# Kernel tuning notes

Measured on AMD Instinct MI355X. Metric: run time of the kernel, lower is better.

Reference implementation:

```python
import jax, jax.numpy as jnp
import numpy as np

B, S, H, DH, W, G, M = 2, 4096, 12, 64, 256, 64, 256
D = H * DH  # 768
VOCAB = 50282
NEG = -1e9


def setup_inputs() -> dict:
    key = jax.random.key(0)
    ks = jax.random.split(key, 16)
    f = lambda k, shp, s=0.02: jax.random.normal(k, shp, jnp.float32) * s
    return {
        'input_ids': jax.random.randint(ks[0], (B, S), 0, VOCAB, jnp.int32),
        'attn_mask': jnp.ones((B, S), jnp.float32),
        'html_idx': jnp.sort(jax.random.randint(ks[1], (B, M), 0, S, jnp.int32), axis=-1),
        'embed': f(ks[2], (VOCAB, D), 1.0),
        'Wq': f(ks[3], (D, D)), 'bq': jnp.zeros((D,), jnp.float32),
        'Wk': f(ks[4], (D, D)), 'bk': jnp.zeros((D,), jnp.float32),
        'Wv': f(ks[5], (D, D)), 'bv': jnp.zeros((D,), jnp.float32),
        'Wo': f(ks[6], (D, D)), 'bo': jnp.zeros((D,), jnp.float32),
        'gamma': jnp.ones((D,), jnp.float32), 'beta': jnp.zeros((D,), jnp.float32),
        'Wp': f(ks[7], (D, D)), 'bp': jnp.zeros((D,), jnp.float32),
        'Wa': f(ks[8], (D, 3)), 'ba': jnp.zeros((3,), jnp.float32),
        'Ws': f(ks[9], (D, 2)), 'bs': jnp.zeros((2,), jnp.float32),
    }


def _band_shift(t, n_chunks):
    # t: [..., n_chunks+2, W, ...chunked along axis -3/-2]; gather 3 neighbor chunks
    return jnp.concatenate([t[..., i:i + n_chunks, :, :] for i in range(3)], axis=-2)


def longformer_hpt(input_ids, attn_mask, html_idx, embed, Wq, bq, Wk, bk, Wv, bv,
                   Wo, bo, gamma, beta, Wp, bp, Wa, ba, Ws, bs):
    x = embed[input_ids]  # [B,S,D]
    heads = lambda t: t.reshape(B, S, H, DH).transpose(0, 2, 1, 3)  # [B,H,S,DH]
    q, k, v = heads(x @ Wq + bq), heads(x @ Wk + bk), heads(x @ Wv + bv)
    scale = 1.0 / np.sqrt(DH).astype(np.float32)
    C = S // W  # chunks

    # --- sliding-window (banded) attention, one-sided window W ---
    kp = jnp.pad(k, ((0, 0), (0, 0), (W, W), (0, 0))).reshape(B, H, C + 2, W, DH)
    vp = jnp.pad(v, ((0, 0), (0, 0), (W, W), (0, 0))).reshape(B, H, C + 2, W, DH)
    k3 = _band_shift(kp, C)  # [B,H,C,3W,DH]
    v3 = _band_shift(vp, C)
    qc = q.reshape(B, H, C, W, DH)
    sb = jnp.einsum('bhcqd,bhckd->bhcqk', qc, k3) * scale  # [B,H,C,W,3W]

    ii = jnp.arange(W)[:, None]
    jj = jnp.arange(3 * W)[None, :]
    band_ok = jnp.abs(jj - W - ii) <= W  # [W,3W]
    keypos = jnp.arange(C)[:, None] * W - W + jnp.arange(3 * W)[None, :]  # [C,3W]
    kvalid = (keypos >= 0) & (keypos < S) & (keypos >= G)  # global keys handled separately
    mp = jnp.pad(attn_mask, ((0, 0), (W, W))).reshape(B, C + 2, W)
    m3 = jnp.concatenate([mp[:, i:i + C] for i in range(3)], axis=2)  # [B,C,3W]
    mask = band_ok[None, :, :] & kvalid[:, None, :] & (m3[:, :, None, :] > 0)[..., :, :].reshape(B, C, 1, 3 * W).astype(bool) if False else (band_ok[None, None, :, :] & kvalid[None, :, None, :] & (m3[:, :, None, :] > 0))  # [B,C,W,3W]
    sb = jnp.where(mask[:, None], sb, NEG).reshape(B, H, S, 3 * W)

    # --- all tokens also attend to the G global tokens ---
    kg, vg = k[:, :, :G], v[:, :, :G]
    sg = jnp.einsum('bhsd,bhgd->bhsg', q, kg) * scale
    sg = jnp.where(attn_mask[:, None, None, :G] > 0, sg, NEG)

    p = jax.nn.softmax(jnp.concatenate([sg, sb], -1), -1)  # [B,H,S,G+3W]
    pg, pb = p[..., :G], p[..., G:].reshape(B, H, C, W, 3 * W)
    out = (jnp.einsum('bhcqk,bhckd->bhcqd', pb, v3).reshape(B, H, S, DH)
           + jnp.einsum('bhsg,bhgd->bhsd', pg, vg))

    # --- global queries attend to everything ---
    sgl = jnp.einsum('bhgd,bhsd->bhgs', q[:, :, :G], k) * scale
    sgl = jnp.where(attn_mask[:, None, None, :] > 0, sgl, NEG)
    outg = jnp.einsum('bhgs,bhsd->bhgd', jax.nn.softmax(sgl, -1), v)
    out = jnp.concatenate([outg, out[:, :, G:]], axis=2)

    ctx = out.transpose(0, 2, 1, 3).reshape(B, S, D)
    h = x + ctx @ Wo + bo
    mu = h.mean(-1, keepdims=True)
    var = ((h - mu) ** 2).mean(-1, keepdims=True)
    hn = (h - mu) / jnp.sqrt(var + 1e-5) * gamma + beta  # last_hidden [B,S,D]

    # probes (ans_probe: Linear(768,3)+Sigmoid, span_probe: Linear(768,2)+Sigmoid)
    ans = jax.nn.sigmoid(hn @ Wa + ba)
    span = jax.nn.sigmoid(hn @ Ws + bs)

    # ReIndexer gather of HTML-element hidden states + ConditionCalculator
    hr = jnp.take_along_axis(hn, html_idx[:, :, None].astype(jnp.int32), axis=1)  # [B,M,D]
    t = jax.nn.relu(hr @ Wp + bp)
    cond = jax.nn.sigmoid(jnp.einsum('bqh,bch->bcq', hr, t))  # [B,M,M]
    return hn, ans, span, cond


def reference(input_ids, attn_mask, html_idx, embed, Wq, bq, Wk, bk, Wv, bv,
              Wo, bo, gamma, beta, Wp, bp, Wa, ba, Ws, bs):
    return longformer_hpt(input_ids, attn_mask, html_idx, embed, Wq, bq, Wk, bk,
                          Wv, bv, Wo, bo, gamma, beta, Wp, bp, Wa, ba, Ws, bs)
```

## Files before the change

### kernel.cpp

```cpp
#include <hip/hip_runtime.h>

typedef unsigned short u16;
typedef unsigned int   u32;
typedef __attribute__((ext_vector_type(8))) short s8v;
typedef __attribute__((ext_vector_type(8))) unsigned short us8;
typedef __attribute__((ext_vector_type(4))) float f4v;

constexpr int BC  = 2;
constexpr int SL  = 4096;
constexpr int NH  = 12;
constexpr int HD  = 64;
constexpr int DM  = 768;
constexpr int WIN = 256;
constexpr int GLB = 64;
constexpr int QN  = 2304;
constexpr int KCH = 16;
constexpr float FOLD = 0.125f * 1.44269504088896f;
constexpr float NEGS = -1.0e9f;

__device__ __forceinline__ float b2f(u16 b){ return __uint_as_float(((u32)b) << 16); }
__device__ __forceinline__ u16 f2b(float f){
  u32 u = __float_as_uint(f);
  return (u16)((u + 0x7fffu + ((u >> 16) & 1u)) >> 16);
}
__device__ __forceinline__ float wredsum(float v){
  #pragma unroll
  for (int o = 32; o > 0; o >>= 1) v += __shfl_xor(v, o, 64);
  return v;
}
__device__ __forceinline__ float sigf(float x){ return 1.f / (1.f + __expf(-x)); }

__global__ void pack_w(const float* __restrict__ Wq, const float* __restrict__ Wk,
                       const float* __restrict__ Wv, const float* __restrict__ Wo,
                       const float* __restrict__ Wp,
                       const float* __restrict__ bq, const float* __restrict__ bk,
                       const float* __restrict__ bv,
                       u16* __restrict__ wt_qkv, u16* __restrict__ wt_o,
                       u16* __restrict__ wt_p, float* __restrict__ b_qkv)
{
  __shared__ float tile[64][65];
  const int bid = blockIdx.x;
  const int mi = bid / 144, rest = bid % 144;
  const int kt = rest / 12, ntc = rest % 12;
  const float* src = (mi==0)?Wq:(mi==1)?Wk:(mi==2)?Wv:(mi==3)?Wo:Wp;
  u16* dst = (mi<3) ? (wt_qkv + (size_t)mi*768*768) : ((mi==3) ? wt_o : wt_p);
  const int t = threadIdx.x;
  const int k0 = kt*64, n0 = ntc*64;
  #pragma unroll
  for (int i=0;i<4;i++){
    const int r = (t>>4) + i*16;
    float4 v = ((const float4*)(src + (long)(k0+r)*768 + n0))[t&15];
    tile[r][(t&15)*4+0] = v.x; tile[r][(t&15)*4+1] = v.y;
    tile[r][(t&15)*4+2] = v.z; tile[r][(t&15)*4+3] = v.w;
  }
  __syncthreads();
  const int n = t & 63, kc = (t>>6)*16;
  u32* d32 = (u32*)(dst + (long)(n0+n)*768 + k0 + kc);
  #pragma unroll
  for (int i=0;i<8;i++){
    d32[i] = (u32)f2b(tile[kc+2*i][n]) | ((u32)f2b(tile[kc+2*i+1][n]) << 16);
  }
  if (bid < 9){
    const int i = bid*256 + t;
    if (i < 2304) b_qkv[i] = (i < 768) ? bq[i] : (i < 1536) ? bk[i-768] : bv[i-1536];
  }
}

__global__ void embed_gather(const int* __restrict__ ids, const float* __restrict__ emb,
                             u16* __restrict__ xb){
  int e4 = blockIdx.x*256 + threadIdx.x;
  if (e4 >= 8192*192) return;
  int row = e4 / 192, d4 = e4 - row*192;
  int id = ids[row];
  float4 v = ((const float4*)(emb + (long)id*768))[d4];
  u32 p0 = (u32)f2b(v.x) | ((u32)f2b(v.y) << 16);
  u32 p1 = (u32)f2b(v.z) | ((u32)f2b(v.w) << 16);
  ((u32*)(xb + (long)row*768))[d4*2]   = p0;
  ((u32*)(xb + (long)row*768))[d4*2+1] = p1;
}

__global__ void gather_hr(const int* __restrict__ hidx, const float* __restrict__ hn,
                          u16* __restrict__ hrb){
  int e = blockIdx.x*256 + threadIdx.x;
  if (e >= 512*768) return;
  int r = e / 768, d = e - r*768;
  int b = r >> 8;
  int idx = hidx[r];
  hrb[e] = f2b(hn[((long)(b*SL + idx))*768 + d]);
}

template<int MODE>
__global__ __launch_bounds__(256, 2)
void gemm_bt(const u16* __restrict__ A, const u16* __restrict__ Bt,
             const float* __restrict__ bias, const u16* __restrict__ resB,
             float* __restrict__ outF, u16* __restrict__ outB,
             int M, int N, int K, long sA, long sB, long sO)
{
  const int bz = blockIdx.z;
  A  += (long)bz * sA;
  Bt += (long)bz * sB;
  const int n0 = blockIdx.x * 128;
  const int m0 = blockIdx.y * 128;
  __shared__ u16 lsA[128*64];
  __shared__ u16 lsB[128*64];
  const int t = threadIdx.x;
  const int w = t >> 6, lane = t & 63;
  const int wr = w >> 1, wc = w & 1;
  const int fr = lane & 15, fq = lane >> 4;

  f4v acc[4][4];
  #pragma unroll
  for (int i=0;i<4;i++)
    #pragma unroll
    for (int j=0;j<4;j++) acc[i][j] = (f4v)0.f;

  for (int k0 = 0; k0 < K; k0 += 64){
    #pragma unroll
    for (int i=0;i<4;i++){
      int e = (w*4+i)*512 + lane*8;
      int row = e >> 6, col = e & 63;
      __builtin_amdgcn_global_load_lds(
        (const __attribute__((address_space(1))) void*)(A + (long)(m0+row)*K + (k0+col)),
        (__attribute__((address_space(3))) void*)(&lsA[(w*4+i)*512]), 16, 0, 0);
      __builtin_amdgcn_global_load_lds(
        (const __attribute__((address_space(1))) void*)(Bt + (long)(n0+row)*K + (k0+col)),
        (__attribute__((address_space(3))) void*)(&lsB[(w*4+i)*512]), 16, 0, 0);
    }
    __syncthreads();
    #pragma unroll
    for (int kk = 0; kk < 2; kk++){
      s8v af[4], bfv[4];
      #pragma unroll
      for (int mi=0;mi<4;mi++)
        af[mi] = *(const s8v*)&lsA[(wr*64 + mi*16 + fr)*64 + kk*32 + fq*8];
      #pragma unroll
      for (int ni=0;ni<4;ni++)
        bfv[ni] = *(const s8v*)&lsB[(wc*64 + ni*16 + fr)*64 + kk*32 + fq*8];
      #pragma unroll
      for (int mi=0;mi<4;mi++)
        #pragma unroll
        for (int ni=0;ni<4;ni++)
          acc[mi][ni] = __builtin_amdgcn_mfma_f32_16x16x32_bf16(af[mi], bfv[ni], acc[mi][ni], 0, 0, 0);
    }
    __syncthreads();
  }
  #pragma unroll
  for (int mi=0;mi<4;mi++){
    #pragma unroll
    for (int ni=0;ni<4;ni++){
      #pragma unroll
      for (int r=0;r<4;r++){
        int row = m0 + wr*64 + mi*16 + fq*4 + r;
        int col = n0 + wc*64 + ni*16 + fr;
        float v = acc[mi][ni][r];
        if constexpr (MODE == 0){
          v += bias[col];
          outB[(long)row*N + col] = f2b(v);
        } else if constexpr (MODE == 1){
          v += bias[col] + b2f(resB[(long)row*N + col]);
          outF[(long)row*N + col] = v;
        } else if constexpr (MODE == 2){
          v = fmaxf(v + bias[col], 0.f);
          outB[(long)row*N + col] = f2b(v);
        } else {
          (outF + bz*sO)[(long)row*N + col] = sigf(v);
        }
      }
    }
  }
}

__global__ __launch_bounds__(256, 3)
void attn_band_mfma(const u16* __restrict__ qkv, const float* __restrict__ mask, u16* __restrict__ ctx)
{
  const int q0 = blockIdx.x * 64;
  const int h = blockIdx.y, b = blockIdx.z;
  const int t = threadIdx.x;
  const int w = t >> 6, lane = t & 63;
  const int fq = lane >> 4, fr = lane & 15;

  __shared__ u16 lsK[2][64*64];
  __shared__ u16 lsVT[2][64*72];
  __shared__ u16 lsP[4][16*72];
  __shared__ float lsM[2][64];

  const long bq = (long)b*SL*QN;
  const u16* qrow = qkv + (bq + (long)(q0 + w*16 + fr)*QN) + h*HD;
  s8v aq[2];
  aq[0] = *(const s8v*)(qrow + fq*8);
  aq[1] = *(const s8v*)(qrow + 32 + fq*8);

  const u16* kq = qkv + bq + DM + h*HD;
  const u16* vq = qkv + bq + 2*DM + h*HD;
  const float* mrow = mask + b*SL;

  const int ti_lo = (q0 < 320) ? ((320 - q0) >> 6) : 0;
  const int ti_hi_raw = (4352 - q0) >> 6;
  const int ti_hi = ti_hi_raw < 9 ? ti_hi_raw : 9;
  const int NTT = 1 + (ti_hi - ti_lo);
  const int kb0 = q0 - 256 + ti_lo*64;

  f4v out[4];
  #pragma unroll
  for (int n=0;n<4;n++) out[n] = (f4v)0.f;
  float m[4]  = {-3.0e38f,-3.0e38f,-3.0e38f,-3.0e38f};
  float l[4]  = {0.f,0.f,0.f,0.f};

  us8 vv0, vv1;
  auto stage_issue = [&](int i, int buf){
    const int k0 = (i == 0) ? 0 : kb0 + (i-1)*64;
    if (t < 64) lsM[buf][t] = mrow[k0 + t];
    #pragma unroll
    for (int j=0;j<2;j++){
      const int r = (w*2+j)*8 + (lane>>3);
      const int d = ((lane&7) ^ (lane>>3))*8;
      __builtin_amdgcn_global_load_lds(
        (const __attribute__((address_space(1))) void*)(kq + (long)(k0+r)*QN + d),
        (__attribute__((address_space(3))) void*)(&lsK[buf][(w*2+j)*512]), 16, 0, 0);
    }
    vv0 = *(const us8*)(vq + (long)(k0+lane)*QN + w*8);
    vv1 = *(const us8*)(vq + (long)(k0+lane)*QN + w*8 + 32);
  };

  stage_issue(0, 0);
  int cur = 0;
  for (int i = 0; i < NTT; i++){
    const int k0 = (i == 0) ? 0 : kb0 + (i-1)*64;
    const int d0 = w*8;
    #pragma unroll
    for (int jj=0;jj<8;jj++) lsVT[cur][(d0+jj)*72 + lane] = (u16)vv0[jj];
    #pragma unroll
    for (int jj=0;jj<8;jj++) lsVT[cur][(d0+32+jj)*72 + lane] = (u16)vv1[jj];
    __syncthreads();
    if (i+1 < NTT) stage_issue(i+1, cur^1);

    f4v s[4];
    #pragma unroll
    for (int n=0;n<4;n++) s[n] = (f4v)0.f;
    #pragma unroll
    for (int kk=0;kk<2;kk++){
      #pragma unroll
      for (int n=0;n<4;n++){
        s8v bf = *(const s8v*)&lsK[cur][(16*n+fr)*64 + (((kk*4+fq) ^ (fr&7))<<3)];
        s[n] = __builtin_amdgcn_mfma_f32_16x16x32_bf16(aq[kk], bf, s[n], 0,0,0);
      }
    }
    const bool isg = (i == 0);
    #pragma unroll
    for (int n=0;n<4;n++){
      const int kcol = 16*n + fr;
      const float mk = lsM[cur][kcol];
      #pragma unroll
      for (int r=0;r<4;r++){
        const int dd = k0 + kcol - (q0 + w*16 + fq*4 + r);
        const bool valid = (mk > 0.f) && (isg || (dd >= -WIN && dd <= WIN));
        s[n][r] = valid ? s[n][r]*FOLD : NEGS;
      }
    }
    float sf[4];
    #pragma unroll
    for (int r=0;r<4;r++){
      float rm = fmaxf(fmaxf(s[0][r], s[1][r]), fmaxf(s[2][r], s[3][r]));
      rm = fmaxf(rm, __shfl_xor(rm, 1, 64));
      rm = fmaxf(rm, __shfl_xor(rm, 2, 64));
      rm = fmaxf(rm, __shfl_xor(rm, 4, 64));
      rm = fmaxf(rm, __shfl_xor(rm, 8, 64));
      const float mn = fmaxf(m[r], rm);
      sf[r] = exp2f(m[r] - mn);
      m[r] = mn;
    }
    u16* lsPw = lsP[w];
    float rs[4] = {0.f,0.f,0.f,0.f};
    #pragma unroll
    for (int n=0;n<4;n++){
      #pragma unroll
      for (int r=0;r<4;r++){
        float p = exp2f(s[n][r] - m[r]);
        rs[r] += p;
        lsPw[(fq*4+r)*72 + 16*n + fr] = f2b(p);
        out[n][r] *= sf[r];
      }
    }
    #pragma unroll
    for (int r=0;r<4;r++){
      float rv = rs[r];
      rv += __shfl_xor(rv, 1, 64);
      rv += __shfl_xor(rv, 2, 64);
      rv += __shfl_xor(rv, 4, 64);
      rv += __shfl_xor(rv, 8, 64);
      l[r] = l[r]*sf[r] + rv;
    }
    s8v ap[2];
    ap[0] = *(const s8v*)&lsPw[fr*72 + fq*8];
    ap[1] = *(const s8v*)&lsPw[fr*72 + 32 + fq*8];
    #pragma unroll
    for (int kk=0;kk<2;kk++){
      #pragma unroll
      for (int n=0;n<4;n++){
        s8v bv = *(const s8v*)&lsVT[cur][(16*n+fr)*72 + kk*32 + fq*8];
        out[n] = __builtin_amdgcn_mfma_f32_16x16x32_bf16(ap[kk], bv, out[n], 0,0,0);
      }
    }
    cur ^= 1;
  }
  #pragma unroll
  for (int r=0;r<4;r++) l[r] = 1.f/l[r];
  u16* cb = ctx + (((long)(b*SL) + q0 + w*16 + fq*4))*DM + h*HD + fr;
  #pragma unroll
  for (int n=0;n<4;n++)
    #pragma unroll
    for (int r=0;r<4;r++)
      cb[(long)r*DM + 16*n] = f2b(out[n][r]*l[r]);
}

__global__ __launch_bounds__(256, 3)
void attn_global_part(const u16* __restrict__ qkv, const float* __restrict__ mask,
                      float* __restrict__ pout, float* __restrict__ pml)
{
  const int ck = blockIdx.x;
  const int h = blockIdx.y, b = blockIdx.z;
  const int bh = b*NH + h;
  const int t = threadIdx.x;
  const int w = t >> 6, lane = t & 63;
  const int fq = lane >> 4, fr = lane & 15;

  __shared__ u16 lsK[2][64*64];
  __shared__ u16 lsVT[2][64*72];
  __shared__ u16 lsP[4][16*72];
  __shared__ float lsM[2][64];

  const long bq = (long)b*SL*QN;
  const u16* qrow = qkv + (bq + (long)(w*16 + fr)*QN) + h*HD;
  s8v aq[2];
  aq[0] = *(const s8v*)(qrow + fq*8);
  aq[1] = *(const s8v*)(qrow + 32 + fq*8);

  const u16* kq = qkv + bq + DM + h*HD;
  const u16* vq = qkv + bq + 2*DM + h*HD;
  const float* mrow = mask + b*SL;

  f4v out[4];
  #pragma unroll
  for (int n=0;n<4;n++) out[n] = (f4v)0.f;
  float m[4]  = {-3.0e38f,-3.0e38f,-3.0e38f,-3.0e38f};
  float l[4]  = {0.f,0.f,0.f,0.f};

  us8 vv0, vv1;
  auto stage_issue = [&](int i, int buf){
    const int k0 = ck*256 + i*64;
    if (t < 64) lsM[buf][t] = mrow[k0 + t];
    #pragma unroll
    for (int j=0;j<2;j++){
      const int r = (w*2+j)*8 + (lane>>3);
      const int d = ((lane&7) ^ (lane>>3))*8;
      __builtin_amdgcn_global_load_lds(
        (const __attribute__((address_space(1))) void*)(kq + (long)(k0+r)*QN + d),
        (__attribute__((address_space(3))) void*)(&lsK[buf][(w*2+j)*512]), 16, 0, 0);
    }
    vv0 = *(const us8*)(vq + (long)(k0+lane)*QN + w*8);
    vv1 = *(const us8*)(vq + (long)(k0+lane)*QN + w*8 + 32);
  };

  stage_issue(0, 0);
  int cur = 0;
  for (int i = 0; i < 4; i++){
    const int d0 = w*8;
    #pragma unroll
    for (int jj=0;jj<8;jj++) lsVT[cur][(d0+jj)*72 + lane] = (u16)vv0[jj];
    #pragma unroll
    for (int jj=0;jj<8;jj++) lsVT[cur][(d0+32+jj)*72 + lane] = (u16)vv1[jj];
    __syncthreads();
    if (i+1 < 4) stage_issue(i+1, cur^1);

    f4v s[4];
    #pragma unroll
    for (int n=0;n<4;n++) s[n] = (f4v)0.f;
    #pragma unroll
    for (int kk=0;kk<2;kk++){
      #pragma unroll
      for (int n=0;n<4;n++){
        s8v bf = *(const s8v*)&lsK[cur][(16*n+fr)*64 + (((kk*4+fq) ^ (fr&7))<<3)];
        s[n] = __builtin_amdgcn_mfma_f32_16x16x32_bf16(aq[kk], bf, s[n], 0,0,0);
      }
    }
    #pragma unroll
    for (int n=0;n<4;n++){
      const float mk = lsM[cur][16*n + fr];
      #pragma unroll
      for (int r=0;r<4;r++)
        s[n][r] = (mk > 0.f) ? s[n][r]*FOLD : NEGS;
    }
    float sf[4];
    #pragma unroll
    for (int r=0;r<4;r++){
      float rm = fmaxf(fmaxf(s[0][r], s[1][r]), fmaxf(s[2][r], s[3][r]));
      rm = fmaxf(rm, __shfl_xor(rm, 1, 64));
      rm = fmaxf(rm, __shfl_xor(rm, 2, 64));
      rm = fmaxf(rm, __shfl_xor(rm, 4, 64));
      rm = fmaxf(rm, __shfl_xor(rm, 8, 64));
      const float mn = fmaxf(m[r], rm);
      sf[r] = exp2f(m[r] - mn);
      m[r] = mn;
    }
    u16* lsPw = lsP[w];
    float rs[4] = {0.f,0.f,0.f,0.f};
    #pragma unroll
    for (int n=0;n<4;n++){
      #pragma unroll
      for (int r=0;r<4;r++){
        float p = exp2f(s[n][r] - m[r]);
        rs[r] += p;
        lsPw[(fq*4+r)*72 + 16*n + fr] = f2b(p);
        out[n][r] *= sf[r];
      }
    }
    #pragma unroll
    for (int r=0;r<4;r++){
      float rv = rs[r];
      rv += __shfl_xor(rv, 1, 64);
      rv += __shfl_xor(rv, 2, 64);
      rv += __shfl_xor(rv, 4, 64);
      rv += __shfl_xor(rv, 8, 64);
      l[r] = l[r]*sf[r] + rv;
    }
    s8v ap[2];
    ap[0] = *(const s8v*)&lsPw[fr*72 + fq*8];
    ap[1] = *(const s8v*)&lsPw[fr*72 + 32 + fq*8];
    #pragma unroll
    for (int kk=0;kk<2;kk++){
      #pragma unroll
      for (int n=0;n<4;n++){
        s8v bv = *(const s8v*)&lsVT[cur][(16*n+fr)*72 + kk*32 + fq*8];
        out[n] = __builtin_amdgcn_mfma_f32_16x16x32_bf16(ap[kk], bv, out[n], 0,0,0);
      }
    }
    cur ^= 1;
  }
  float* pob = pout + ((long)(ck*BC*NH + bh))*64*64;
  #pragma unroll
  for (int n=0;n<4;n++)
    #pragma unroll
    for (int r=0;r<4;r++)
      pob[(w*16 + fq*4 + r)*64 + 16*n + fr] = out[n][r];
  if (fr == 0){
    float* pmb = pml + ((long)(ck*BC*NH + bh))*128;
    #pragma unroll
    for (int r=0;r<4;r++){
      pmb[(w*16 + fq*4 + r)*2 + 0] = m[r];
      pmb[(w*16 + fq*4 + r)*2 + 1] = l[r];
    }
  }
}

__global__ __launch_bounds__(256, 2)
void attn_global_combine(const float* __restrict__ pout, const float* __restrict__ pml,
                         u16* __restrict__ ctx)
{
  const int bh = blockIdx.x;
  const int b = bh / NH, h = bh % NH;
  const int t = threadIdx.x;
  __shared__ float wgt[KCH][64];
  __shared__ float rl[64];
  if (t < 64){
    float mc[KCH], lc[KCH];
    #pragma unroll
    for (int c = 0; c < KCH; c++){
      const float* pmb = pml + ((long)(c*BC*NH + bh))*128 + t*2;
      mc[c] = pmb[0]; lc[c] = pmb[1];
    }
    float M = mc[0];
    #pragma unroll
    for (int c = 1; c < KCH; c++) M = fmaxf(M, mc[c]);
    float L = 0.f;
    #pragma unroll
    for (int c = 0; c < KCH; c++){
      const float wv = exp2f(mc[c] - M);
      wgt[c][t] = wv;
      L += lc[c]*wv;
    }
    rl[t] = 1.f/L;
  }
  __syncthreads();
  const int row = t >> 2, dseg = t & 3;
  float acc[16];
  #pragma unroll
  for (int i=0;i<16;i++) acc[i] = 0.f;
  for (int c = 0; c < KCH; c++){
    const float wv = wgt[c][row];
    const float4* pb = (const float4*)(pout + ((long)(c*BC*NH + bh)*64 + row)*64 + dseg*16);
    #pragma unroll
    for (int i = 0; i < 4; i++){
      float4 v = pb[i];
      acc[i*4+0] += v.x*wv; acc[i*4+1] += v.y*wv;
      acc[i*4+2] += v.z*wv; acc[i*4+3] += v.w*wv;
    }
  }
  u16* cr = ctx + ((long)(b*SL + row))*DM + h*HD + dseg*16;
  const float r = rl[row];
  #pragma unroll
  for (int i = 0; i < 16; i += 2){
    u32 pk = (u32)f2b(acc[i]*r) | ((u32)f2b(acc[i+1]*r) << 16);
    *(u32*)(cr + i) = pk;
  }
}

__global__ __launch_bounds__(256, 2)
void ln_heads(const float* __restrict__ hbuf, const float* __restrict__ gamma, const float* __restrict__ beta,
              const float* __restrict__ Wa, const float* __restrict__ ba,
              const float* __restrict__ Wsp, const float* __restrict__ bsp,
              float* __restrict__ hn, float* __restrict__ ans, float* __restrict__ span)
{
  const int r = blockIdx.x;
  const int t = threadIdx.x, lane = t & 63, w = t >> 6;
  __shared__ float red[8];
  __shared__ float dred[4][5];
  const float* hrow = hbuf + (long)r*DM;
  float v0 = hrow[t], v1 = hrow[t+256], v2 = hrow[t+512];
  float sum = wredsum(v0 + v1 + v2);
  float sq  = wredsum(v0*v0 + v1*v1 + v2*v2);
  if (lane == 0){ red[w] = sum; red[4+w] = sq; }
  __syncthreads();
  const float mu  = (red[0]+red[1]+red[2]+red[3]) * (1.f/768.f);
  const float msq = (red[4]+red[5]+red[6]+red[7]) * (1.f/768.f);
  const float rstd = rsqrtf(msq - mu*mu + 1e-5f);
  float pa0=0,pa1=0,pa2=0,ps0=0,ps1=0;
  const long base = (long)r*DM;
  #pragma unroll
  for (int jj = 0; jj < 3; jj++){
    const int i = t + jj*256;
    const float hv = (jj==0) ? v0 : (jj==1) ? v1 : v2;
    const float y = (hv - mu)*rstd*gamma[i] + beta[i];
    hn[base + i] = y;
    pa0 += y*Wa[i*3+0]; pa1 += y*Wa[i*3+1]; pa2 += y*Wa[i*3+2];
    ps0 += y*Wsp[i*2+0]; ps1 += y*Wsp[i*2+1];
  }
  pa0 = wredsum(pa0); pa1 = wredsum(pa1); pa2 = wredsum(pa2);
  ps0 = wredsum(ps0); ps1 = wredsum(ps1);
  if (lane == 0){ dred[w][0]=pa0; dred[w][1]=pa1; dred[w][2]=pa2; dred[w][3]=ps0; dred[w][4]=ps1; }
  __syncthreads();
  if (t == 0){
    float A0 = dred[0][0]+dred[1][0]+dred[2][0]+dred[3][0];
    float A1 = dred[0][1]+dred[1][1]+dred[2][1]+dred[3][1];
    float A2 = dred[0][2]+dred[1][2]+dred[2][2]+dred[3][2];
    float S0 = dred[0][3]+dred[1][3]+dred[2][3]+dred[3][3];
    float S1 = dred[0][4]+dred[1][4]+dred[2][4]+dred[3][4];
    ans[(long)r*3+0]  = sigf(A0 + ba[0]);
    ans[(long)r*3+1]  = sigf(A1 + ba[1]);
    ans[(long)r*3+2]  = sigf(A2 + ba[2]);
    span[(long)r*2+0] = sigf(S0 + bsp[0]);
    span[(long)r*2+1] = sigf(S1 + bsp[1]);
  }
}

extern "C" void kernel_launch(void* const* d_in, const int* in_sizes, int n_in,
                              void* d_out, int out_size, void* d_ws, size_t ws_size,
                              hipStream_t stream)
{
  const int*   input_ids = (const int*)  d_in[0];
  const float* attn_mask = (const float*)d_in[1];
  const int*   html_idx  = (const int*)  d_in[2];
  const float* embed     = (const float*)d_in[3];
  const float* Wq = (const float*)d_in[4];  const float* bq = (const float*)d_in[5];
  const float* Wk = (const float*)d_in[6];  const float* bk = (const float*)d_in[7];
  const float* Wv = (const float*)d_in[8];  const float* bv = (const float*)d_in[9];
  const float* Wo = (const float*)d_in[10]; const float* bo = (const float*)d_in[11];
  const float* gamma = (const float*)d_in[12]; const float* beta = (const float*)d_in[13];
  const float* Wp = (const float*)d_in[14]; const float* bp = (const float*)d_in[15];
  const float* Wa = (const float*)d_in[16]; const float* ba = (const float*)d_in[17];
  const float* Wsp = (const float*)d_in[18]; const float* bsp = (const float*)d_in[19];

  char* ws = (char*)d_ws;
  size_t off = 0;
  auto take = [&](size_t bytes)->char*{
    char* p = ws + off; off += (bytes + 255) & ~(size_t)255; return p;
  };
  u16*   x_b    = (u16*)  take((size_t)8192*768*2);
  u16*   wt_qkv = (u16*)  take((size_t)2304*768*2);
  u16*   wt_o   = (u16*)  take((size_t)768*768*2);
  u16*   wt_p   = (u16*)  take((size_t)768*768*2);
  float* b_qkv  = (float*)take(2304*4);
  u16*   qkv_b  = (u16*)  take((size_t)8192*2304*2);
  u16*   ctx_b  = (u16*)  take((size_t)8192*768*2);
  float* h_f    = (float*)take((size_t)8192*768*4);
  u16*   hr_b   = (u16*)  take((size_t)512*768*2);
  u16*   t_b    = (u16*)  take((size_t)512*768*2);
  float* pout   = (float*)take((size_t)KCH*BC*NH*64*64*4);
  float* pml    = (float*)take((size_t)KCH*BC*NH*128*4);

  float* out_hn   = (float*)d_out;
  float* out_ans  = out_hn  + (size_t)8192*768;
  float* out_span = out_ans + (size_t)8192*3;
  float* out_cond = out_span + (size_t)8192*2;

  pack_w<<<720, 256, 0, stream>>>(Wq, Wk, Wv, Wo, Wp, bq, bk, bv,
                                  wt_qkv, wt_o, wt_p, b_qkv);
  embed_gather<<<6144, 256, 0, stream>>>(input_ids, embed, x_b);

  gemm_bt<0><<<dim3(18,64,1), 256, 0, stream>>>(x_b, wt_qkv, b_qkv, nullptr,
                                                nullptr, qkv_b, 8192, 2304, 768, 0,0,0);
  attn_band_mfma<<<dim3(64,12,2), 256, 0, stream>>>(qkv_b, attn_mask, ctx_b);
  attn_global_part<<<dim3(KCH,12,2), 256, 0, stream>>>(qkv_b, attn_mask, pout, pml);
  attn_global_combine<<<BC*NH, 256, 0, stream>>>(pout, pml, ctx_b);
  gemm_bt<1><<<dim3(6,64,1), 256, 0, stream>>>(ctx_b, wt_o, bo, x_b,
                                               h_f, nullptr, 8192, 768, 768, 0,0,0);
  ln_heads<<<8192, 256, 0, stream>>>(h_f, gamma, beta, Wa, ba, Wsp, bsp,
                                     out_hn, out_ans, out_span);
  gather_hr<<<1536, 256, 0, stream>>>(html_idx, out_hn, hr_b);
  gemm_bt<2><<<dim3(6,4,1), 256, 0, stream>>>(hr_b, wt_p, bp, nullptr,
                                              nullptr, t_b, 512, 768, 768, 0,0,0);
  gemm_bt<3><<<dim3(2,2,2), 256, 0, stream>>>(t_b, hr_b, nullptr, nullptr,
                                              out_cond, nullptr, 256, 256, 768,
                                              (long)256*768, (long)256*768, (long)256*256);
}
```

Before: 234.5 us.

## Widen band-attention blocks, lazy softmax rescale, swizzle GEMMs, fuse pack and embed

The banded attention kernel now uses 512-thread blocks covering 128 queries, so each staged K/V tile serves eight waves. It also visits query blocks in a permuted order, raises wave priority around the MFMA sections, and rescales the running softmax state only when the row max grows by more than a threshold. The global-attention split doubles its chunk count so each block handles fewer key tiles. The large GEMMs get a grid-swizzle remapping of block IDs, and weight packing and the embedding gather are merged into one launch. The changes cut launches and redundant K/V loads and trade that for higher register and shared-memory pressure, plus more partials to combine.

```diff
diff --git a/kernel.cpp b/kernel.cpp
--- a/kernel.cpp
+++ b/kernel.cpp
@@ -14,7 +14,7 @@
 constexpr int WIN = 256;
 constexpr int GLB = 64;
 constexpr int QN  = 2304;
-constexpr int KCH = 16;
+constexpr int KCH = 32;
 constexpr float FOLD = 0.125f * 1.44269504088896f;
 constexpr float NEGS = -1.0e9f;
 
@@ -30,53 +30,53 @@
 }
 __device__ __forceinline__ float sigf(float x){ return 1.f / (1.f + __expf(-x)); }
 
-__global__ void pack_w(const float* __restrict__ Wq, const float* __restrict__ Wk,
-                       const float* __restrict__ Wv, const float* __restrict__ Wo,
-                       const float* __restrict__ Wp,
-                       const float* __restrict__ bq, const float* __restrict__ bk,
-                       const float* __restrict__ bv,
-                       u16* __restrict__ wt_qkv, u16* __restrict__ wt_o,
-                       u16* __restrict__ wt_p, float* __restrict__ b_qkv)
+__global__ void pack_embed(const float* __restrict__ Wq, const float* __restrict__ Wk,
+                           const float* __restrict__ Wv, const float* __restrict__ Wo,
+                           const float* __restrict__ Wp,
+                           const float* __restrict__ bq, const float* __restrict__ bk,
+                           const float* __restrict__ bv,
+                           u16* __restrict__ wt_qkv, u16* __restrict__ wt_o,
+                           u16* __restrict__ wt_p, float* __restrict__ b_qkv,
+                           const int* __restrict__ ids, const float* __restrict__ emb,
+                           u16* __restrict__ xb)
 {
   __shared__ float tile[64][65];
   const int bid = blockIdx.x;
-  const int mi = bid / 144, rest = bid % 144;
-  const int kt = rest / 12, ntc = rest % 12;
-  const float* src = (mi==0)?Wq:(mi==1)?Wk:(mi==2)?Wv:(mi==3)?Wo:Wp;
-  u16* dst = (mi<3) ? (wt_qkv + (size_t)mi*768*768) : ((mi==3) ? wt_o : wt_p);
   const int t = threadIdx.x;
-  const int k0 = kt*64, n0 = ntc*64;
-  #pragma unroll
-  for (int i=0;i<4;i++){
-    const int r = (t>>4) + i*16;
-    float4 v = ((const float4*)(src + (long)(k0+r)*768 + n0))[t&15];
-    tile[r][(t&15)*4+0] = v.x; tile[r][(t&15)*4+1] = v.y;
-    tile[r][(t&15)*4+2] = v.z; tile[r][(t&15)*4+3] = v.w;
-  }
-  __syncthreads();
-  const int n = t & 63, kc = (t>>6)*16;
-  u32* d32 = (u32*)(dst + (long)(n0+n)*768 + k0 + kc);
-  #pragma unroll
-  for (int i=0;i<8;i++){
-    d32[i] = (u32)f2b(tile[kc+2*i][n]) | ((u32)f2b(tile[kc+2*i+1][n]) << 16);
-  }
-  if (bid < 9){
-    const int i = bid*256 + t;
-    if (i < 2304) b_qkv[i] = (i < 768) ? bq[i] : (i < 1536) ? bk[i-768] : bv[i-1536];
-  }
-}
-
-__global__ void embed_gather(const int* __restrict__ ids, const float* __restrict__ emb,
-                             u16* __restrict__ xb){
-  int e4 = blockIdx.x*256 + threadIdx.x;
-  if (e4 >= 8192*192) return;
-  int row = e4 / 192, d4 = e4 - row*192;
-  int id = ids[row];
-  float4 v = ((const float4*)(emb + (long)id*768))[d4];
-  u32 p0 = (u32)f2b(v.x) | ((u32)f2b(v.y) << 16);
-  u32 p1 = (u32)f2b(v.z) | ((u32)f2b(v.w) << 16);
-  ((u32*)(xb + (long)row*768))[d4*2]   = p0;
-  ((u32*)(xb + (long)row*768))[d4*2+1] = p1;
+  if (bid < 720){
+    const int mi = bid / 144, rest = bid % 144;
+    const int kt = rest / 12, ntc = rest % 12;
+    const float* src = (mi==0)?Wq:(mi==1)?Wk:(mi==2)?Wv:(mi==3)?Wo:Wp;
+    u16* dst = (mi<3) ? (wt_qkv + (size_t)mi*768*768) : ((mi==3) ? wt_o : wt_p);
+    const int k0 = kt*64, n0 = ntc*64;
+    #pragma unroll
+    for (int i=0;i<4;i++){
+      const int r = (t>>4) + i*16;
+      float4 v = ((const float4*)(src + (long)(k0+r)*768 + n0))[t&15];
+      tile[r][(t&15)*4+0] = v.x; tile[r][(t&15)*4+1] = v.y;
+      tile[r][(t&15)*4+2] = v.z; tile[r][(t&15)*4+3] = v.w;
+    }
+    __syncthreads();
+    const int n = t & 63, kc = (t>>6)*16;
+    u32* d32 = (u32*)(dst + (long)(n0+n)*768 + k0 + kc);
+    #pragma unroll
+    for (int i=0;i<8;i++){
+      d32[i] = (u32)f2b(tile[kc+2*i][n]) | ((u32)f2b(tile[kc+2*i+1][n]) << 16);
+    }
+    if (bid < 9){
+      const int i = bid*256 + t;
+      if (i < 2304) b_qkv[i] = (i < 768) ? bq[i] : (i < 1536) ? bk[i-768] : bv[i-1536];
+    }
+  } else {
+    int e4 = (bid-720)*256 + t;
+    int row = e4 / 192, d4 = e4 - row*192;
+    int id = ids[row];
+    float4 v = ((const float4*)(emb + (long)id*768))[d4];
+    u32 p0 = (u32)f2b(v.x) | ((u32)f2b(v.y) << 16);
+    u32 p1 = (u32)f2b(v.z) | ((u32)f2b(v.w) << 16);
+    ((u32*)(xb + (long)row*768))[d4*2]   = p0;
+    ((u32*)(xb + (long)row*768))[d4*2+1] = p1;
+  }
 }
 
 __global__ void gather_hr(const int* __restrict__ hidx, const float* __restrict__ hn,
@@ -89,7 +89,7 @@
   hrb[e] = f2b(hn[((long)(b*SL + idx))*768 + d]);
 }
 
-template<int MODE>
+template<int MODE, bool SWZ>
 __global__ __launch_bounds__(256, 2)
 void gemm_bt(const u16* __restrict__ A, const u16* __restrict__ Bt,
              const float* __restrict__ bias, const u16* __restrict__ resB,
@@ -99,8 +99,13 @@
   const int bz = blockIdx.z;
   A  += (long)bz * sA;
   Bt += (long)bz * sB;
-  const int n0 = blockIdx.x * 128;
-  const int m0 = blockIdx.y * 128;
+  int vid = blockIdx.x + gridDim.x*blockIdx.y;
+  if constexpr (SWZ){
+    const int chunk = (gridDim.x*gridDim.y) >> 3;
+    vid = (vid & 7)*chunk + (vid >> 3);
+  }
+  const int n0 = (vid % gridDim.x) * 128;
+  const int m0 = (vid / gridDim.x) * 128;
   __shared__ u16 lsA[128*64];
   __shared__ u16 lsB[128*64];
   const int t = threadIdx.x;
@@ -170,22 +175,24 @@
   }
 }
 
-__global__ __launch_bounds__(256, 3)
+__global__ __launch_bounds__(512, 2)
 void attn_band_mfma(const u16* __restrict__ qkv, const float* __restrict__ mask, u16* __restrict__ ctx)
 {
-  const int q0 = blockIdx.x * 64;
+  const int bx = blockIdx.x;
+  const int q0 = (((bx & 7) << 2) | (bx >> 3)) * 128;
   const int h = blockIdx.y, b = blockIdx.z;
   const int t = threadIdx.x;
   const int w = t >> 6, lane = t & 63;
   const int fq = lane >> 4, fr = lane & 15;
+  const int qw = ((w >> 2) << 6) | ((w & 3) << 4);
 
   __shared__ u16 lsK[2][64*64];
   __shared__ u16 lsVT[2][64*72];
-  __shared__ u16 lsP[4][16*72];
+  __shared__ u16 lsP[8][16*72];
   __shared__ float lsM[2][64];
 
   const long bq = (long)b*SL*QN;
-  const u16* qrow = qkv + (bq + (long)(q0 + w*16 + fr)*QN) + h*HD;
+  const u16* qrow = qkv + (bq + (long)(q0 + qw + fr)*QN) + h*HD;
   s8v aq[2];
   aq[0] = *(const s8v*)(qrow + fq*8);
   aq[1] = *(const s8v*)(qrow + 32 + fq*8);
@@ -194,11 +201,9 @@
   const u16* vq = qkv + bq + 2*DM + h*HD;
   const float* mrow = mask + b*SL;
 
-  const int ti_lo = (q0 < 320) ? ((320 - q0) >> 6) : 0;
-  const int ti_hi_raw = (4352 - q0) >> 6;
-  const int ti_hi = ti_hi_raw < 9 ? ti_hi_raw : 9;
-  const int NTT = 1 + (ti_hi - ti_lo);
-  const int kb0 = q0 - 256 + ti_lo*64;
+  const int kb0 = (q0 < 320) ? 64 : (q0 - 256);
+  const int khi = (q0 + 384 < SL) ? (q0 + 384) : SL;
+  const int NTT = 1 + ((khi - kb0) >> 6);
 
   f4v out[4];
   #pragma unroll
@@ -206,20 +211,16 @@
   float m[4]  = {-3.0e38f,-3.0e38f,-3.0e38f,-3.0e38f};
   float l[4]  = {0.f,0.f,0.f,0.f};
 
-  us8 vv0, vv1;
+  us8 vv;
   auto stage_issue = [&](int i, int buf){
     const int k0 = (i == 0) ? 0 : kb0 + (i-1)*64;
     if (t < 64) lsM[buf][t] = mrow[k0 + t];
-    #pragma unroll
-    for (int j=0;j<2;j++){
-      const int r = (w*2+j)*8 + (lane>>3);
-      const int d = ((lane&7) ^ (lane>>3))*8;
-      __builtin_amdgcn_global_load_lds(
-        (const __attribute__((address_space(1))) void*)(kq + (long)(k0+r)*QN + d),
-        (__attribute__((address_space(3))) void*)(&lsK[buf][(w*2+j)*512]), 16, 0, 0);
-    }
-    vv0 = *(const us8*)(vq + (long)(k0+lane)*QN + w*8);
-    vv1 = *(const us8*)(vq + (long)(k0+lane)*QN + w*8 + 32);
+    const int r = w*8 + (lane>>3);
+    const int d = ((lane&7) ^ (lane>>3))*8;
+    __builtin_amdgcn_global_load_lds(
+      (const __attribute__((address_space(1))) void*)(kq + (long)(k0+r)*QN + d),
+      (__attribute__((address_space(3))) void*)(&lsK[buf][w*512]), 16, 0, 0);
+    vv = *(const us8*)(vq + (long)(k0+lane)*QN + w*8);
   };
 
   stage_issue(0, 0);
@@ -228,15 +229,14 @@
     const int k0 = (i == 0) ? 0 : kb0 + (i-1)*64;
     const int d0 = w*8;
     #pragma unroll
-    for (int jj=0;jj<8;jj++) lsVT[cur][(d0+jj)*72 + lane] = (u16)vv0[jj];
-    #pragma unroll
-    for (int jj=0;jj<8;jj++) lsVT[cur][(d0+32+jj)*72 + lane] = (u16)vv1[jj];
+    for (int jj=0;jj<8;jj++) lsVT[cur][(d0+jj)*72 + lane] = (u16)vv[jj];
     __syncthreads();
     if (i+1 < NTT) stage_issue(i+1, cur^1);
 
     f4v s[4];
     #pragma unroll
     for (int n=0;n<4;n++) s[n] = (f4v)0.f;
+    __builtin_amdgcn_s_setprio(1);
     #pragma unroll
     for (int kk=0;kk<2;kk++){
       #pragma unroll
@@ -245,6 +245,7 @@
         s[n] = __builtin_amdgcn_mfma_f32_16x16x32_bf16(aq[kk], bf, s[n], 0,0,0);
       }
     }
+    __builtin_amdgcn_s_setprio(0);
     const bool isg = (i == 0);
     #pragma unroll
     for (int n=0;n<4;n++){
@@ -252,22 +253,34 @@
       const float mk = lsM[cur][kcol];
       #pragma unroll
       for (int r=0;r<4;r++){
-        const int dd = k0 + kcol - (q0 + w*16 + fq*4 + r);
+        const int dd = k0 + kcol - (q0 + qw + fq*4 + r);
         const bool valid = (mk > 0.f) && (isg || (dd >= -WIN && dd <= WIN));
         s[n][r] = valid ? s[n][r]*FOLD : NEGS;
       }
     }
-    float sf[4];
+    float rm[4];
     #pragma unroll
     for (int r=0;r<4;r++){
-      float rm = fmaxf(fmaxf(s[0][r], s[1][r]), fmaxf(s[2][r], s[3][r]));
-      rm = fmaxf(rm, __shfl_xor(rm, 1, 64));
-      rm = fmaxf(rm, __shfl_xor(rm, 2, 64));
-      rm = fmaxf(rm, __shfl_xor(rm, 4, 64));
-      rm = fmaxf(rm, __shfl_xor(rm, 8, 64));
-      const float mn = fmaxf(m[r], rm);
-      sf[r] = exp2f(m[r] - mn);
-      m[r] = mn;
+      float v = fmaxf(fmaxf(s[0][r], s[1][r]), fmaxf(s[2][r], s[3][r]));
+      v = fmaxf(v, __shfl_xor(v, 1, 64));
+      v = fmaxf(v, __shfl_xor(v, 2, 64));
+      v = fmaxf(v, __shfl_xor(v, 4, 64));
+      v = fmaxf(v, __shfl_xor(v, 8, 64));
+      rm[r] = v;
+    }
+    bool need = false;
+    #pragma unroll
+    for (int r=0;r<4;r++) need |= (rm[r] > m[r] + 8.f);
+    if (__any(need)){
+      #pragma unroll
+      for (int r=0;r<4;r++){
+        const float mn = fmaxf(m[r], rm[r]);
+        const float sf = exp2f(m[r] - mn);
+        m[r] = mn;
+        l[r] *= sf;
+        #pragma unroll
+        for (int n=0;n<4;n++) out[n][r] *= sf;
+      }
     }
     u16* lsPw = lsP[w];
     float rs[4] = {0.f,0.f,0.f,0.f};
@@ -278,7 +291,6 @@
         float p = exp2f(s[n][r] - m[r]);
         rs[r] += p;
         lsPw[(fq*4+r)*72 + 16*n + fr] = f2b(p);
-        out[n][r] *= sf[r];
       }
     }
     #pragma unroll
@@ -288,11 +300,12 @@
       rv += __shfl_xor(rv, 2, 64);
       rv += __shfl_xor(rv, 4, 64);
       rv += __shfl_xor(rv, 8, 64);
-      l[r] = l[r]*sf[r] + rv;
+      l[r] += rv;
     }
     s8v ap[2];
     ap[0] = *(const s8v*)&lsPw[fr*72 + fq*8];
     ap[1] = *(const s8v*)&lsPw[fr*72 + 32 + fq*8];
+    __builtin_amdgcn_s_setprio(1);
     #pragma unroll
     for (int kk=0;kk<2;kk++){
       #pragma unroll
@@ -301,11 +314,12 @@
         out[n] = __builtin_amdgcn_mfma_f32_16x16x32_bf16(ap[kk], bv, out[n], 0,0,0);
       }
     }
+    __builtin_amdgcn_s_setprio(0);
     cur ^= 1;
   }
   #pragma unroll
   for (int r=0;r<4;r++) l[r] = 1.f/l[r];
-  u16* cb = ctx + (((long)(b*SL) + q0 + w*16 + fq*4))*DM + h*HD + fr;
+  u16* cb = ctx + (((long)(b*SL) + q0 + qw + fq*4))*DM + h*HD + fr;
   #pragma unroll
   for (int n=0;n<4;n++)
     #pragma unroll
@@ -347,7 +361,7 @@
 
   us8 vv0, vv1;
   auto stage_issue = [&](int i, int buf){
-    const int k0 = ck*256 + i*64;
+    const int k0 = ck*128 + i*64;
     if (t < 64) lsM[buf][t] = mrow[k0 + t];
     #pragma unroll
     for (int j=0;j<2;j++){
@@ -363,18 +377,19 @@
 
   stage_issue(0, 0);
   int cur = 0;
-  for (int i = 0; i < 4; i++){
+  for (int i = 0; i < 2; i++){
     const int d0 = w*8;
     #pragma unroll
     for (int jj=0;jj<8;jj++) lsVT[cur][(d0+jj)*72 + lane] = (u16)vv0[jj];
     #pragma unroll
     for (int jj=0;jj<8;jj++) lsVT[cur][(d0+32+jj)*72 + lane] = (u16)vv1[jj];
     __syncthreads();
-    if (i+1 < 4) stage_issue(i+1, cur^1);
+    if (i+1 < 2) stage_issue(i+1, cur^1);
 
     f4v s[4];
     #pragma unroll
     for (int n=0;n<4;n++) s[n] = (f4v)0.f;
+    __builtin_amdgcn_s_setprio(1);
     #pragma unroll
     for (int kk=0;kk<2;kk++){
       #pragma unroll
@@ -383,6 +398,7 @@
         s[n] = __builtin_amdgcn_mfma_f32_16x16x32_bf16(aq[kk], bf, s[n], 0,0,0);
       }
     }
+    __builtin_amdgcn_s_setprio(0);
     #pragma unroll
     for (int n=0;n<4;n++){
       const float mk = lsM[cur][16*n + fr];
@@ -426,6 +442,7 @@
     s8v ap[2];
     ap[0] = *(const s8v*)&lsPw[fr*72 + fq*8];
     ap[1] = *(const s8v*)&lsPw[fr*72 + 32 + fq*8];
+    __builtin_amdgcn_s_setprio(1);
     #pragma unroll
     for (int kk=0;kk<2;kk++){
       #pragma unroll
@@ -434,6 +451,7 @@
         out[n] = __builtin_amdgcn_mfma_f32_16x16x32_bf16(ap[kk], bv, out[n], 0,0,0);
       }
     }
+    __builtin_amdgcn_s_setprio(0);
     cur ^= 1;
   }
   float* pob = pout + ((long)(ck*BC*NH + bh))*64*64;
@@ -592,23 +610,23 @@
   float* out_span = out_ans + (size_t)8192*3;
   float* out_cond = out_span + (size_t)8192*2;
 
-  pack_w<<<720, 256, 0, stream>>>(Wq, Wk, Wv, Wo, Wp, bq, bk, bv,
-                                  wt_qkv, wt_o, wt_p, b_qkv);
-  embed_gather<<<6144, 256, 0, stream>>>(input_ids, embed, x_b);
-
-  gemm_bt<0><<<dim3(18,64,1), 256, 0, stream>>>(x_b, wt_qkv, b_qkv, nullptr,
+  pack_embed<<<6864, 256, 0, stream>>>(Wq, Wk, Wv, Wo, Wp, bq, bk, bv,
+                                       wt_qkv, wt_o, wt_p, b_qkv,
+                                       input_ids, embed, x_b);
+
+  gemm_bt<0,true><<<dim3(18,64,1), 256, 0, stream>>>(x_b, wt_qkv, b_qkv, nullptr,
                                                 nullptr, qkv_b, 8192, 2304, 768, 0,0,0);
-  attn_band_mfma<<<dim3(64,12,2), 256, 0, stream>>>(qkv_b, attn_mask, ctx_b);
+  attn_band_mfma<<<dim3(32,12,2), 512, 0, stream>>>(qkv_b, attn_mask, ctx_b);
   attn_global_part<<<dim3(KCH,12,2), 256, 0, stream>>>(qkv_b, attn_mask, pout, pml);
   attn_global_combine<<<BC*NH, 256, 0, stream>>>(pout, pml, ctx_b);
-  gemm_bt<1><<<dim3(6,64,1), 256, 0, stream>>>(ctx_b, wt_o, bo, x_b,
+  gemm_bt<1,true><<<dim3(6,64,1), 256, 0, stream>>>(ctx_b, wt_o, bo, x_b,
                                                h_f, nullptr, 8192, 768, 768, 0,0,0);
   ln_heads<<<8192, 256, 0, stream>>>(h_f, gamma, beta, Wa, ba, Wsp, bsp,
                                      out_hn, out_ans, out_span);
   gather_hr<<<1536, 256, 0, stream>>>(html_idx, out_hn, hr_b);
-  gemm_bt<2><<<dim3(6,4,1), 256, 0, stream>>>(hr_b, wt_p, bp, nullptr,
+  gemm_bt<2,false><<<dim3(6,4,1), 256, 0, stream>>>(hr_b, wt_p, bp, nullptr,
                                               nullptr, t_b, 512, 768, 768, 0,0,0);
-  gemm_bt<3><<<dim3(2,2,2), 256, 0, stream>>>(t_b, hr_b, nullptr, nullptr,
+  gemm_bt<3,false><<<dim3(2,2,2), 256, 0, stream>>>(t_b, hr_b, nullptr, nullptr,
                                               out_cond, nullptr, 256, 256, 768,
                                               (long)256*768, (long)256*768, (long)256*256);
 }
```

New measurement: 235.1 us. No clear change (+0.2%).
